# Kernel optimization log

Hardware: AMD Instinct MI355X
Metric: run time of the kernel (lower is better)

The kernel has to match this reference:

```python
import jax, jax.numpy as jnp
import numpy as np

D = 512
E = 1024
LAMBDA_INIT = 0.05

def setup_inputs() -> dict:
    key = jax.random.key(0)
    ks = jax.random.split(key, 8)
    B, S = 4, 4096
    X = jax.random.normal(ks[0], (B, S, E), dtype=jnp.float32)
    Wq = jax.random.normal(ks[1], (2 * D, E), dtype=jnp.float32) / np.sqrt(E)
    bq = jnp.zeros((2 * D,), dtype=jnp.float32)
    Wk = jax.random.normal(ks[2], (2 * D, E), dtype=jnp.float32) / np.sqrt(E)
    bk = jnp.zeros((2 * D,), dtype=jnp.float32)
    Wv = jax.random.normal(ks[3], (D, E), dtype=jnp.float32) / np.sqrt(E)
    bv = jnp.zeros((D,), dtype=jnp.float32)
    lam = jax.random.normal(ks[4], (1,), dtype=jnp.float32)
    return {"X": X, "Wq": Wq, "bq": bq, "Wk": Wk, "bk": bk, "Wv": Wv, "bv": bv, "lam": lam}

def reference(X, Wq, bq, Wk, bk, Wv, bv, lam):
    # Linear projections (torch Linear: x @ W.T + b)
    Q = jnp.einsum('bse,fe->bsf', X, Wq) + bq   # [B,S,2d]
    K = jnp.einsum('bse,fe->bsf', X, Wk) + bk   # [B,S,2d]
    V = jnp.einsum('bse,de->bsd', X, Wv) + bv   # [B,S,d]
    Q1, Q2 = Q[..., :D], Q[..., D:]
    K1, K2 = K[..., :D], K[..., D:]
    s = 1.0 / np.sqrt(D)
    A1 = jnp.einsum('bqd,bkd->bqk', Q1, K1) * s  # [B,S,S]
    A2 = jnp.einsum('bqd,bkd->bqk', Q2, K2) * s
    P1 = jax.nn.softmax(A1, axis=-1)
    P2 = jax.nn.softmax(A2, axis=-1)
    lambda_ = jnp.exp(lam) + LAMBDA_INIT         # scalar [1]
    diff = P1 - lambda_ * P2
    return jnp.einsum('bqk,bkd->bqd', diff, V)   # [B,S,d]
```

## Files before the change

### kernel.cpp

```cpp
#include <hip/hip_runtime.h>
#include <cstdint>
#include <cstddef>

#define NB    4
#define SEQ   4096
#define EDIM  1024
#define DHEAD 512
#define NTOK  (NB * SEQ)
#define FQK   2048
#define FQKV  2560

typedef __bf16 bf16x8 __attribute__((ext_vector_type(8)));
typedef float  f32x4  __attribute__((ext_vector_type(4)));

__device__ __forceinline__ unsigned short f2bf(float f) {
  union { float f; unsigned int u; } v; v.f = f;
  return (unsigned short)((v.u + 0x7fffu + ((v.u >> 16) & 1u)) >> 16);
}
__device__ __forceinline__ float bf2f(unsigned short h) {
  union { unsigned int u; float f; } v; v.u = ((unsigned int)h) << 16;
  return v.f;
}

__device__ __forceinline__ void gld_lds16(const void* g, void* l) {
  __builtin_amdgcn_global_load_lds(
      (const __attribute__((address_space(1))) unsigned int*)g,
      (__attribute__((address_space(3))) unsigned int*)l, 16, 0, 0);
}

template <class Epi>
__device__ __forceinline__ void gemm_bt_core(
    const unsigned short* __restrict__ A, const unsigned short* __restrict__ B,
    int K, int lda, int ldb, int m0, int n0, Epi epi) {
  __shared__ __align__(16) unsigned short As[128 * 32];
  __shared__ __align__(16) unsigned short Bs[128 * 32];
  const int t = threadIdx.x;
  const int w = t >> 6;
  const int lane = t & 63;
  const int wr = w >> 1, wc = w & 1;

  f32x4 acc[4][4];
#pragma unroll
  for (int i = 0; i < 4; ++i)
#pragma unroll
    for (int j = 0; j < 4; ++j) acc[i][j] = f32x4{0.f, 0.f, 0.f, 0.f};

  const int c0 = (w * 2) * 64 + lane;
  const int c1 = (w * 2 + 1) * 64 + lane;
  const int r0 = c0 >> 2, col0 = (c0 & 3) * 8;
  const int r1 = c1 >> 2, col1 = (c1 & 3) * 8;
  unsigned short* ldsA0 = &As[(w * 2) * 512];
  unsigned short* ldsA1 = &As[(w * 2 + 1) * 512];
  unsigned short* ldsB0 = &Bs[(w * 2) * 512];
  unsigned short* ldsB1 = &Bs[(w * 2 + 1) * 512];
  const unsigned short* gA0 = A + (size_t)(m0 + r0) * lda + col0;
  const unsigned short* gA1 = A + (size_t)(m0 + r1) * lda + col1;
  const unsigned short* gB0 = B + (size_t)(n0 + r0) * ldb + col0;
  const unsigned short* gB1 = B + (size_t)(n0 + r1) * ldb + col1;

  for (int kt = 0; kt < K; kt += 32) {
    gld_lds16(gA0 + kt, ldsA0);
    gld_lds16(gA1 + kt, ldsA1);
    gld_lds16(gB0 + kt, ldsB0);
    gld_lds16(gB1 + kt, ldsB1);
    __syncthreads();

    bf16x8 af[4], bfr[4];
#pragma unroll
    for (int tm = 0; tm < 4; ++tm) {
      int r = wr * 64 + tm * 16 + (lane & 15);
      af[tm] = *(const bf16x8*)&As[r * 32 + (lane >> 4) * 8];
    }
#pragma unroll
    for (int tn = 0; tn < 4; ++tn) {
      int r = wc * 64 + tn * 16 + (lane & 15);
      bfr[tn] = *(const bf16x8*)&Bs[r * 32 + (lane >> 4) * 8];
    }
#pragma unroll
    for (int tm = 0; tm < 4; ++tm)
#pragma unroll
      for (int tn = 0; tn < 4; ++tn)
        acc[tm][tn] = __builtin_amdgcn_mfma_f32_16x16x32_bf16(
            af[tm], bfr[tn], acc[tm][tn], 0, 0, 0);
    __syncthreads();
  }
  epi(acc, wr, wc, lane);
}

__global__ void k_cvt_x(const float* __restrict__ X, unsigned short* __restrict__ Xb) {
  int i = blockIdx.x * blockDim.x + threadIdx.x;
  float4 v = ((const float4*)X)[i];
  ushort4 o;
  o.x = f2bf(v.x); o.y = f2bf(v.y); o.z = f2bf(v.z); o.w = f2bf(v.w);
  ((ushort4*)Xb)[i] = o;
}

__global__ void k_pack_w(const float* __restrict__ Wq, const float* __restrict__ Wk,
                         const float* __restrict__ Wv, unsigned short* __restrict__ Wb) {
  int i = blockIdx.x * blockDim.x + threadIdx.x;
  int idx = i * 4;
  int f = idx >> 10, e = idx & 1023;
  const float* src = (f < 1024) ? (Wq + (size_t)f * 1024)
                   : (f < 2048) ? (Wk + (size_t)(f - 1024) * 1024)
                                : (Wv + (size_t)(f - 2048) * 1024);
  float4 v = *(const float4*)(src + e);
  ushort4 o;
  o.x = f2bf(v.x); o.y = f2bf(v.y); o.z = f2bf(v.z); o.w = f2bf(v.w);
  ((ushort4*)Wb)[i] = o;
}

__global__ void k_pack_b(const float* __restrict__ bq, const float* __restrict__ bk,
                         const float* __restrict__ bv, float* __restrict__ bc) {
  int f = blockIdx.x * blockDim.x + threadIdx.x;
  if (f < FQKV)
    bc[f] = (f < 1024) ? bq[f] : (f < 2048) ? bk[f - 1024] : bv[f - 2048];
}

__global__ void k_zero_f(float* __restrict__ p) {
  int i = blockIdx.x * blockDim.x + threadIdx.x;
  p[i] = 0.f;
}

__global__ __launch_bounds__(256) void k_qk(const unsigned short* __restrict__ Xb,
                                            const unsigned short* __restrict__ Wb,
                                            const float* __restrict__ bc,
                                            unsigned short* __restrict__ QK) {
  __shared__ __align__(16) unsigned short Ps[128 * 136];
  const int m0 = blockIdx.y * 128, n0 = blockIdx.x * 128;
  gemm_bt_core(Xb, Wb, EDIM, EDIM, EDIM, m0, n0,
    [&](f32x4 (&acc)[4][4], int wr, int wc, int lane) {
      const int w = wr * 2 + wc;
#pragma unroll
      for (int tm = 0; tm < 4; ++tm)
#pragma unroll
        for (int tn = 0; tn < 4; ++tn) {
          int kc = wc * 64 + tn * 16 + (lane & 15);
          float bias = bc[n0 + kc];
#pragma unroll
          for (int i = 0; i < 4; ++i) {
            int ql = wr * 64 + tm * 16 + (lane >> 4) * 4 + i;
            Ps[ql * 136 + kc] = f2bf(acc[tm][tn][i] + bias);
          }
        }
      __syncthreads();
#pragma unroll
      for (int j = 0; j < 8; ++j) {
        int row = w * 32 + j * 4 + (lane >> 4);
        int col = (lane & 15) * 8;
        uint4 v = *(const uint4*)&Ps[row * 136 + col];
        *(uint4*)&QK[(size_t)(m0 + row) * FQK + n0 + col] = v;
      }
    });
}

__global__ __launch_bounds__(256) void k_v(const unsigned short* __restrict__ Xb,
                                           const unsigned short* __restrict__ Wb,
                                           const float* __restrict__ bc,
                                           unsigned short* __restrict__ Vt) {
  const int b = blockIdx.z;
  const int m0 = blockIdx.y * 128;
  const int n0 = blockIdx.x * 128;
  const unsigned short* A = Wb + (size_t)2048 * EDIM;
  const unsigned short* B = Xb + (size_t)b * SEQ * EDIM;
  unsigned short* Vb = Vt + (size_t)b * DHEAD * SEQ;
  gemm_bt_core(A, B, EDIM, EDIM, EDIM, m0, n0,
    [&](f32x4 (&acc)[4][4], int wr, int wc, int lane) {
#pragma unroll
      for (int tm = 0; tm < 4; ++tm)
#pragma unroll
        for (int tn = 0; tn < 4; ++tn) {
          int s = n0 + wc * 64 + tn * 16 + (lane & 15);
#pragma unroll
          for (int i = 0; i < 4; ++i) {
            int d = m0 + wr * 64 + tm * 16 + (lane >> 4) * 4 + i;
            Vb[(size_t)d * SEQ + s] = f2bf(acc[tm][tn][i] + bc[2048 + d]);
          }
        }
    });
}

__global__ __launch_bounds__(512) void k_scores3(const unsigned short* __restrict__ QK,
                                                 unsigned short* __restrict__ E_c,
                                                 float* __restrict__ ls, int b0) {
  __shared__ __align__(16) unsigned short As[256 * 32];
  __shared__ __align__(16) unsigned short Bs[128 * 32];
  const int z = blockIdx.z;
  const int rb = z >> 1, which = z & 1;
  const int b = b0 + rb;
  const int m0 = blockIdx.y * 256;
  const int n0 = blockIdx.x * 128;
  const unsigned short* Aq = QK + (size_t)b * SEQ * FQK + which * 512;
  const unsigned short* Bk = QK + (size_t)b * SEQ * FQK + 1024 + which * 512;
  unsigned short* Eb = E_c + (size_t)z * SEQ * SEQ;
  float* lr = ls + (size_t)which * NTOK + (size_t)b * SEQ;
  const int t = threadIdx.x, w = t >> 6, lane = t & 63;
  const int wr = w >> 1, wc = w & 1;

  f32x4 acc[4][4];
#pragma unroll
  for (int i = 0; i < 4; ++i)
#pragma unroll
    for (int j = 0; j < 4; ++j) acc[i][j] = f32x4{0.f, 0.f, 0.f, 0.f};

  const int cA0 = w * 128 + lane;
  const int cA1 = w * 128 + 64 + lane;
  const int cB  = w * 64 + lane;
  const unsigned short* gA0 = Aq + (size_t)(m0 + (cA0 >> 2)) * FQK + (cA0 & 3) * 8;
  const unsigned short* gA1 = Aq + (size_t)(m0 + (cA1 >> 2)) * FQK + (cA1 & 3) * 8;
  const unsigned short* gB  = Bk + (size_t)(n0 + (cB >> 2)) * FQK + (cB & 3) * 8;
  unsigned short* ldsA0 = As + (w * 128) * 8;
  unsigned short* ldsA1 = As + (w * 128 + 64) * 8;
  unsigned short* ldsB  = Bs + (w * 64) * 8;

  for (int kt = 0; kt < 512; kt += 32) {
    gld_lds16(gA0 + kt, ldsA0);
    gld_lds16(gA1 + kt, ldsA1);
    gld_lds16(gB + kt, ldsB);
    __syncthreads();

    bf16x8 af[4], bfr[4];
#pragma unroll
    for (int tm = 0; tm < 4; ++tm) {
      int r = wr * 64 + tm * 16 + (lane & 15);
      af[tm] = *(const bf16x8*)&As[r * 32 + (lane >> 4) * 8];
    }
#pragma unroll
    for (int tn = 0; tn < 4; ++tn) {
      int r = wc * 64 + tn * 16 + (lane & 15);
      bfr[tn] = *(const bf16x8*)&Bs[r * 32 + (lane >> 4) * 8];
    }
#pragma unroll
    for (int tm = 0; tm < 4; ++tm)
#pragma unroll
      for (int tn = 0; tn < 4; ++tn)
        acc[tm][tn] = __builtin_amdgcn_mfma_f32_16x16x32_bf16(
            af[tm], bfr[tn], acc[tm][tn], 0, 0, 0);
    __syncthreads();
  }

  const float scale = 0.04419417382415922f;
  float rs[4][4];
#pragma unroll
  for (int tm = 0; tm < 4; ++tm)
#pragma unroll
    for (int i = 0; i < 4; ++i) rs[tm][i] = 0.f;
#pragma unroll
  for (int tm = 0; tm < 4; ++tm)
#pragma unroll
    for (int tn = 0; tn < 4; ++tn) {
      int k = n0 + wc * 64 + tn * 16 + (lane & 15);
#pragma unroll
      for (int i = 0; i < 4; ++i) {
        int q = m0 + wr * 64 + tm * 16 + (lane >> 4) * 4 + i;
        float e = __expf(acc[tm][tn][i] * scale);
        unsigned short eb = f2bf(e);
        Eb[(size_t)q * SEQ + k] = eb;
        rs[tm][i] += bf2f(eb);
      }
    }
#pragma unroll
  for (int tm = 0; tm < 4; ++tm)
#pragma unroll
    for (int i = 0; i < 4; ++i) {
      float v = rs[tm][i];
      v += __shfl_xor(v, 1);
      v += __shfl_xor(v, 2);
      v += __shfl_xor(v, 4);
      v += __shfl_xor(v, 8);
      rs[tm][i] = v;
    }
  if ((lane & 15) == 0) {
#pragma unroll
    for (int tm = 0; tm < 4; ++tm)
#pragma unroll
      for (int i = 0; i < 4; ++i) {
        int q = m0 + wr * 64 + tm * 16 + (lane >> 4) * 4 + i;
        atomicAdd(&lr[q], rs[tm][i]);
      }
  }
}

__global__ __launch_bounds__(256) void k_pv4(const unsigned short* __restrict__ E_c,
                                             const unsigned short* __restrict__ Vt,
                                             float* __restrict__ O12, int b0) {
  __shared__ __align__(16) unsigned short As[64 * 32];
  __shared__ __align__(16) unsigned short Bs[256 * 32];
  const int bid = blockIdx.x;
  const int z = (bid >> 1) & 3;
  const int e = (bid & 1) | ((bid >> 3) << 1);
  const int q0 = (e >> 1) * 64;
  const int n0 = (e & 1) * 256;
  const int b = b0 + (z >> 1);
  const unsigned short* A = E_c + (size_t)z * SEQ * SEQ;
  const unsigned short* Bv = Vt + (size_t)b * DHEAD * SEQ;
  float* Ob = O12 + (size_t)z * SEQ * DHEAD;
  const int t = threadIdx.x, w = t >> 6, lane = t & 63;

  f32x4 acc[4][4];
#pragma unroll
  for (int i = 0; i < 4; ++i)
#pragma unroll
    for (int j = 0; j < 4; ++j) acc[i][j] = f32x4{0.f, 0.f, 0.f, 0.f};

  const int ca = w * 64 + lane;
  const unsigned short* gA = A + (size_t)(q0 + (ca >> 2)) * SEQ + (ca & 3) * 8;
  unsigned short* ldsA = As + (w * 64) * 8;
  const unsigned short* gB[4];
  unsigned short* ldsB[4];
#pragma unroll
  for (int g = 0; g < 4; ++g) {
    int c = w * 256 + g * 64 + lane;
    gB[g] = Bv + (size_t)(n0 + (c >> 2)) * SEQ + (c & 3) * 8;
    ldsB[g] = Bs + (w * 256 + g * 64) * 8;
  }

  for (int kt = 0; kt < SEQ; kt += 32) {
    gld_lds16(gA + kt, ldsA);
#pragma unroll
    for (int g = 0; g < 4; ++g) gld_lds16(gB[g] + kt, ldsB[g]);
    __syncthreads();

    bf16x8 af[4], bfr[4];
#pragma unroll
    for (int tm = 0; tm < 4; ++tm) {
      int r = tm * 16 + (lane & 15);
      af[tm] = *(const bf16x8*)&As[r * 32 + (lane >> 4) * 8];
    }
#pragma unroll
    for (int tn = 0; tn < 4; ++tn) {
      int r = w * 64 + tn * 16 + (lane & 15);
      bfr[tn] = *(const bf16x8*)&Bs[r * 32 + (lane >> 4) * 8];
    }
#pragma unroll
    for (int tm = 0; tm < 4; ++tm)
#pragma unroll
      for (int tn = 0; tn < 4; ++tn)
        acc[tm][tn] = __builtin_amdgcn_mfma_f32_16x16x32_bf16(
            af[tm], bfr[tn], acc[tm][tn], 0, 0, 0);
    __syncthreads();
  }

#pragma unroll
  for (int tm = 0; tm < 4; ++tm)
#pragma unroll
    for (int tn = 0; tn < 4; ++tn) {
      int d = n0 + w * 64 + tn * 16 + (lane & 15);
#pragma unroll
      for (int i = 0; i < 4; ++i) {
        int q = q0 + tm * 16 + (lane >> 4) * 4 + i;
        Ob[(size_t)q * DHEAD + d] = acc[tm][tn][i];
      }
    }
}

__global__ void k_combine(const float* __restrict__ O12, const float* __restrict__ ls,
                          const float* __restrict__ lam, float* __restrict__ out, int b0) {
  int i = blockIdx.x * blockDim.x + threadIdx.x;
  float lambda = expf(lam[0]) + 0.05f;
  int gq = i >> 7;
  int rb = gq >> 12;
  int q = gq & 4095;
  int dv = i & 127;
  int b = b0 + rb;
  float inv1 = 1.f / ls[(size_t)b * SEQ + q];
  float inv2 = lambda / ls[NTOK + (size_t)b * SEQ + q];
  size_t ai = (size_t)(rb * 2) * (SEQ * 128) + (size_t)q * 128 + dv;
  float4 a = ((const float4*)O12)[ai];
  float4 c = ((const float4*)O12)[ai + SEQ * 128];
  float4 r;
  r.x = a.x * inv1 - c.x * inv2;
  r.y = a.y * inv1 - c.y * inv2;
  r.z = a.z * inv1 - c.z * inv2;
  r.w = a.w * inv1 - c.w * inv2;
  ((float4*)out)[(size_t)(b * SEQ + q) * 128 + dv] = r;
}

extern "C" void kernel_launch(void* const* d_in, const int* in_sizes, int n_in,
                              void* d_out, int out_size, void* d_ws, size_t ws_size,
                              hipStream_t stream) {
  const float* X   = (const float*)d_in[0];
  const float* Wq  = (const float*)d_in[1];
  const float* bq  = (const float*)d_in[2];
  const float* Wk  = (const float*)d_in[3];
  const float* bk  = (const float*)d_in[4];
  const float* Wv  = (const float*)d_in[5];
  const float* bv  = (const float*)d_in[6];
  const float* lam = (const float*)d_in[7];
  float* out = (float*)d_out;

  char* ws = (char*)d_ws;
  size_t off = 0;
  auto alloc = [&](size_t b) { size_t r = off; off += (b + 255) & ~(size_t)255; return r; };
  unsigned short* Xb  = (unsigned short*)(ws + alloc((size_t)NTOK * EDIM * 2));
  unsigned short* Wb  = (unsigned short*)(ws + alloc((size_t)FQKV * EDIM * 2));
  float*          bc  = (float*)(ws + alloc((size_t)FQKV * 4));
  unsigned short* QK  = (unsigned short*)(ws + alloc((size_t)NTOK * FQK * 2));
  unsigned short* Vt  = (unsigned short*)(ws + alloc((size_t)NB * DHEAD * SEQ * 2));
  unsigned short* E_c = (unsigned short*)(ws + alloc((size_t)4 * SEQ * SEQ * 2));
  float*          ls  = (float*)(ws + alloc((size_t)2 * NTOK * 4));
  float* O12 = (float*)Xb;

  k_cvt_x<<<dim3((NTOK * EDIM / 4) / 256), dim3(256), 0, stream>>>(X, Xb);
  k_pack_w<<<dim3((FQKV * EDIM / 4) / 256), dim3(256), 0, stream>>>(Wq, Wk, Wv, Wb);
  k_pack_b<<<dim3(10), dim3(256), 0, stream>>>(bq, bk, bv, bc);
  k_qk<<<dim3(FQK / 128, NTOK / 128), dim3(256), 0, stream>>>(Xb, Wb, bc, QK);
  k_v<<<dim3(SEQ / 128, DHEAD / 128, NB), dim3(256), 0, stream>>>(Xb, Wb, bc, Vt);
  k_zero_f<<<dim3(2 * NTOK / 256), dim3(256), 0, stream>>>(ls);
  for (int b0 = 0; b0 < NB; b0 += 2) {
    k_scores3<<<dim3(SEQ / 128, SEQ / 256, 4), dim3(512), 0, stream>>>(QK, E_c, ls, b0);
    k_pv4<<<dim3(512), dim3(256), 0, stream>>>(E_c, Vt, O12, b0);
    k_combine<<<dim3((2 * SEQ * DHEAD / 4) / 256), dim3(256), 0, stream>>>(O12, ls, lam, out, b0);
  }

  (void)in_sizes; (void)n_in; (void)out_size; (void)ws_size;
}
```

Measured before the change: 749.5 us.

## Double-buffer LDS tiles in GEMM kernels and store QK directly

Converts the GEMM mainloops (shared core, scores, PV) to a two-stage LDS ping-pong: the next k-tile's global-to-LDS loads are issued before computing on the current tile, removing one barrier per iteration and overlapping memory with MFMA. The QK projection epilogue drops its LDS staging buffer and writes bf16 results directly to global memory. This doubles LDS usage, which can lower occupancy, and the direct epilogue uses narrow uncoalesced stores.

```diff
diff --git a/kernel.cpp b/kernel.cpp
--- a/kernel.cpp
+++ b/kernel.cpp
@@ -32,8 +32,8 @@
 __device__ __forceinline__ void gemm_bt_core(
     const unsigned short* __restrict__ A, const unsigned short* __restrict__ B,
     int K, int lda, int ldb, int m0, int n0, Epi epi) {
-  __shared__ __align__(16) unsigned short As[128 * 32];
-  __shared__ __align__(16) unsigned short Bs[128 * 32];
+  __shared__ __align__(16) unsigned short As[2][128 * 32];
+  __shared__ __align__(16) unsigned short Bs[2][128 * 32];
   const int t = threadIdx.x;
   const int w = t >> 6;
   const int lane = t & 63;
@@ -49,32 +49,38 @@
   const int c1 = (w * 2 + 1) * 64 + lane;
   const int r0 = c0 >> 2, col0 = (c0 & 3) * 8;
   const int r1 = c1 >> 2, col1 = (c1 & 3) * 8;
-  unsigned short* ldsA0 = &As[(w * 2) * 512];
-  unsigned short* ldsA1 = &As[(w * 2 + 1) * 512];
-  unsigned short* ldsB0 = &Bs[(w * 2) * 512];
-  unsigned short* ldsB1 = &Bs[(w * 2 + 1) * 512];
+  const int o0 = (w * 2) * 512;
+  const int o1 = (w * 2 + 1) * 512;
   const unsigned short* gA0 = A + (size_t)(m0 + r0) * lda + col0;
   const unsigned short* gA1 = A + (size_t)(m0 + r1) * lda + col1;
   const unsigned short* gB0 = B + (size_t)(n0 + r0) * ldb + col0;
   const unsigned short* gB1 = B + (size_t)(n0 + r1) * ldb + col1;
 
+  gld_lds16(gA0, &As[0][o0]);
+  gld_lds16(gA1, &As[0][o1]);
+  gld_lds16(gB0, &Bs[0][o0]);
+  gld_lds16(gB1, &Bs[0][o1]);
+  __syncthreads();
+
+  int cur = 0;
   for (int kt = 0; kt < K; kt += 32) {
-    gld_lds16(gA0 + kt, ldsA0);
-    gld_lds16(gA1 + kt, ldsA1);
-    gld_lds16(gB0 + kt, ldsB0);
-    gld_lds16(gB1 + kt, ldsB1);
-    __syncthreads();
-
+    const int nxt = cur ^ 1;
+    if (kt + 32 < K) {
+      gld_lds16(gA0 + kt + 32, &As[nxt][o0]);
+      gld_lds16(gA1 + kt + 32, &As[nxt][o1]);
+      gld_lds16(gB0 + kt + 32, &Bs[nxt][o0]);
+      gld_lds16(gB1 + kt + 32, &Bs[nxt][o1]);
+    }
     bf16x8 af[4], bfr[4];
 #pragma unroll
     for (int tm = 0; tm < 4; ++tm) {
       int r = wr * 64 + tm * 16 + (lane & 15);
-      af[tm] = *(const bf16x8*)&As[r * 32 + (lane >> 4) * 8];
+      af[tm] = *(const bf16x8*)&As[cur][r * 32 + (lane >> 4) * 8];
     }
 #pragma unroll
     for (int tn = 0; tn < 4; ++tn) {
       int r = wc * 64 + tn * 16 + (lane & 15);
-      bfr[tn] = *(const bf16x8*)&Bs[r * 32 + (lane >> 4) * 8];
+      bfr[tn] = *(const bf16x8*)&Bs[cur][r * 32 + (lane >> 4) * 8];
     }
 #pragma unroll
     for (int tm = 0; tm < 4; ++tm)
@@ -83,6 +89,7 @@
         acc[tm][tn] = __builtin_amdgcn_mfma_f32_16x16x32_bf16(
             af[tm], bfr[tn], acc[tm][tn], 0, 0, 0);
     __syncthreads();
+    cur = nxt;
   }
   epi(acc, wr, wc, lane);
 }
@@ -125,31 +132,21 @@
                                             const unsigned short* __restrict__ Wb,
                                             const float* __restrict__ bc,
                                             unsigned short* __restrict__ QK) {
-  __shared__ __align__(16) unsigned short Ps[128 * 136];
   const int m0 = blockIdx.y * 128, n0 = blockIdx.x * 128;
   gemm_bt_core(Xb, Wb, EDIM, EDIM, EDIM, m0, n0,
     [&](f32x4 (&acc)[4][4], int wr, int wc, int lane) {
-      const int w = wr * 2 + wc;
 #pragma unroll
       for (int tm = 0; tm < 4; ++tm)
 #pragma unroll
         for (int tn = 0; tn < 4; ++tn) {
-          int kc = wc * 64 + tn * 16 + (lane & 15);
-          float bias = bc[n0 + kc];
+          int kc = n0 + wc * 64 + tn * 16 + (lane & 15);
+          float bias = bc[kc];
 #pragma unroll
           for (int i = 0; i < 4; ++i) {
-            int ql = wr * 64 + tm * 16 + (lane >> 4) * 4 + i;
-            Ps[ql * 136 + kc] = f2bf(acc[tm][tn][i] + bias);
+            int q = m0 + wr * 64 + tm * 16 + (lane >> 4) * 4 + i;
+            QK[(size_t)q * FQK + kc] = f2bf(acc[tm][tn][i] + bias);
           }
         }
-      __syncthreads();
-#pragma unroll
-      for (int j = 0; j < 8; ++j) {
-        int row = w * 32 + j * 4 + (lane >> 4);
-        int col = (lane & 15) * 8;
-        uint4 v = *(const uint4*)&Ps[row * 136 + col];
-        *(uint4*)&QK[(size_t)(m0 + row) * FQK + n0 + col] = v;
-      }
     });
 }
 
@@ -182,8 +179,8 @@
 __global__ __launch_bounds__(512) void k_scores3(const unsigned short* __restrict__ QK,
                                                  unsigned short* __restrict__ E_c,
                                                  float* __restrict__ ls, int b0) {
-  __shared__ __align__(16) unsigned short As[256 * 32];
-  __shared__ __align__(16) unsigned short Bs[128 * 32];
+  __shared__ __align__(16) unsigned short As[2][256 * 32];
+  __shared__ __align__(16) unsigned short Bs[2][128 * 32];
   const int z = blockIdx.z;
   const int rb = z >> 1, which = z & 1;
   const int b = b0 + rb;
@@ -208,26 +205,33 @@
   const unsigned short* gA0 = Aq + (size_t)(m0 + (cA0 >> 2)) * FQK + (cA0 & 3) * 8;
   const unsigned short* gA1 = Aq + (size_t)(m0 + (cA1 >> 2)) * FQK + (cA1 & 3) * 8;
   const unsigned short* gB  = Bk + (size_t)(n0 + (cB >> 2)) * FQK + (cB & 3) * 8;
-  unsigned short* ldsA0 = As + (w * 128) * 8;
-  unsigned short* ldsA1 = As + (w * 128 + 64) * 8;
-  unsigned short* ldsB  = Bs + (w * 64) * 8;
-
+  const int oA0 = (w * 128) * 8;
+  const int oA1 = (w * 128 + 64) * 8;
+  const int oB  = (w * 64) * 8;
+
+  gld_lds16(gA0, &As[0][oA0]);
+  gld_lds16(gA1, &As[0][oA1]);
+  gld_lds16(gB,  &Bs[0][oB]);
+  __syncthreads();
+
+  int cur = 0;
   for (int kt = 0; kt < 512; kt += 32) {
-    gld_lds16(gA0 + kt, ldsA0);
-    gld_lds16(gA1 + kt, ldsA1);
-    gld_lds16(gB + kt, ldsB);
-    __syncthreads();
-
+    const int nxt = cur ^ 1;
+    if (kt + 32 < 512) {
+      gld_lds16(gA0 + kt + 32, &As[nxt][oA0]);
+      gld_lds16(gA1 + kt + 32, &As[nxt][oA1]);
+      gld_lds16(gB + kt + 32,  &Bs[nxt][oB]);
+    }
     bf16x8 af[4], bfr[4];
 #pragma unroll
     for (int tm = 0; tm < 4; ++tm) {
       int r = wr * 64 + tm * 16 + (lane & 15);
-      af[tm] = *(const bf16x8*)&As[r * 32 + (lane >> 4) * 8];
+      af[tm] = *(const bf16x8*)&As[cur][r * 32 + (lane >> 4) * 8];
     }
 #pragma unroll
     for (int tn = 0; tn < 4; ++tn) {
       int r = wc * 64 + tn * 16 + (lane & 15);
-      bfr[tn] = *(const bf16x8*)&Bs[r * 32 + (lane >> 4) * 8];
+      bfr[tn] = *(const bf16x8*)&Bs[cur][r * 32 + (lane >> 4) * 8];
     }
 #pragma unroll
     for (int tm = 0; tm < 4; ++tm)
@@ -236,6 +240,7 @@
         acc[tm][tn] = __builtin_amdgcn_mfma_f32_16x16x32_bf16(
             af[tm], bfr[tn], acc[tm][tn], 0, 0, 0);
     __syncthreads();
+    cur = nxt;
   }
 
   const float scale = 0.04419417382415922f;
@@ -283,8 +288,8 @@
 __global__ __launch_bounds__(256) void k_pv4(const unsigned short* __restrict__ E_c,
                                              const unsigned short* __restrict__ Vt,
                                              float* __restrict__ O12, int b0) {
-  __shared__ __align__(16) unsigned short As[64 * 32];
-  __shared__ __align__(16) unsigned short Bs[256 * 32];
+  __shared__ __align__(16) unsigned short As[2][64 * 32];
+  __shared__ __align__(16) unsigned short Bs[2][256 * 32];
   const int bid = blockIdx.x;
   const int z = (bid >> 1) & 3;
   const int e = (bid & 1) | ((bid >> 3) << 1);
@@ -304,32 +309,39 @@
 
   const int ca = w * 64 + lane;
   const unsigned short* gA = A + (size_t)(q0 + (ca >> 2)) * SEQ + (ca & 3) * 8;
-  unsigned short* ldsA = As + (w * 64) * 8;
+  const int oA = (w * 64) * 8;
   const unsigned short* gB[4];
-  unsigned short* ldsB[4];
+  int oB[4];
 #pragma unroll
   for (int g = 0; g < 4; ++g) {
     int c = w * 256 + g * 64 + lane;
     gB[g] = Bv + (size_t)(n0 + (c >> 2)) * SEQ + (c & 3) * 8;
-    ldsB[g] = Bs + (w * 256 + g * 64) * 8;
-  }
-
+    oB[g] = (w * 256 + g * 64) * 8;
+  }
+
+  gld_lds16(gA, &As[0][oA]);
+#pragma unroll
+  for (int g = 0; g < 4; ++g) gld_lds16(gB[g], &Bs[0][oB[g]]);
+  __syncthreads();
+
+  int cur = 0;
   for (int kt = 0; kt < SEQ; kt += 32) {
-    gld_lds16(gA + kt, ldsA);
-#pragma unroll
-    for (int g = 0; g < 4; ++g) gld_lds16(gB[g] + kt, ldsB[g]);
-    __syncthreads();
-
+    const int nxt = cur ^ 1;
+    if (kt + 32 < SEQ) {
+      gld_lds16(gA + kt + 32, &As[nxt][oA]);
+#pragma unroll
+      for (int g = 0; g < 4; ++g) gld_lds16(gB[g] + kt + 32, &Bs[nxt][oB[g]]);
+    }
     bf16x8 af[4], bfr[4];
 #pragma unroll
     for (int tm = 0; tm < 4; ++tm) {
       int r = tm * 16 + (lane & 15);
-      af[tm] = *(const bf16x8*)&As[r * 32 + (lane >> 4) * 8];
+      af[tm] = *(const bf16x8*)&As[cur][r * 32 + (lane >> 4) * 8];
     }
 #pragma unroll
     for (int tn = 0; tn < 4; ++tn) {
       int r = w * 64 + tn * 16 + (lane & 15);
-      bfr[tn] = *(const bf16x8*)&Bs[r * 32 + (lane >> 4) * 8];
+      bfr[tn] = *(const bf16x8*)&Bs[cur][r * 32 + (lane >> 4) * 8];
     }
 #pragma unroll
     for (int tm = 0; tm < 4; ++tm)
@@ -338,6 +350,7 @@
         acc[tm][tn] = __builtin_amdgcn_mfma_f32_16x16x32_bf16(
             af[tm], bfr[tn], acc[tm][tn], 0, 0, 0);
     __syncthreads();
+    cur = nxt;
   }
 
 #pragma unroll
```

Result: faster. 719.9 us (-4.0%).
